# Performance work log

Measured on AMD Instinct MI355X. Metric: run time of the kernel, lower is better.

The kernel has to match this reference:

```python
import jax, jax.numpy as jnp
import numpy as np

N, E, IN, HID, H, G = 50000, 400000, 128, 16, 11, 64
HC = HID * H  # 176
OUT, NC = 32, 10
EPS = 1e-5


def setup_inputs() -> dict:
    key = jax.random.key(0)
    ks = jax.random.split(key, 20)
    def n(i, shape, s=0.05):
        return jax.random.normal(ks[i], shape, jnp.float32) * s
    inp = {}
    inp["x"] = jax.random.normal(ks[0], (N, IN), jnp.float32)
    inp["edge_index"] = jax.random.randint(ks[1], (2, E), 0, N, dtype=jnp.int32)
    inp["batch"] = jnp.sort(jax.random.randint(ks[2], (N,), 0, G, dtype=jnp.int32))
    inp["W_pre"] = n(3, (IN, HC)); inp["b_pre"] = jnp.zeros((HC,), jnp.float32)
    # GraphNorm params for gn_pre, gn1..gn4 stacked: [5, HC]
    inp["gn_w"] = jnp.ones((5, HC), jnp.float32)
    inp["gn_b"] = jnp.zeros((5, HC), jnp.float32)
    inp["gn_ms"] = jnp.ones((5, HC), jnp.float32)  # mean_scale
    # conv1..conv4 (concat=True) stacked params
    inp["conv_Wl"] = n(4, (4, HC, HC)); inp["conv_Wr"] = n(5, (4, HC, HC))
    inp["conv_att"] = n(6, (4, H, HID))
    inp["conv_b"] = jnp.zeros((4, HC), jnp.float32)
    inp["conv_Wres"] = n(7, (4, HC, HC))
    # conv5 (concat=False -> out dim HID)
    inp["c5_Wl"] = n(8, (HC, HC)); inp["c5_Wr"] = n(9, (HC, HC))
    inp["c5_att"] = n(10, (H, HID))
    inp["c5_b"] = jnp.zeros((HID,), jnp.float32)
    inp["c5_Wres"] = n(11, (HC, HID))
    inp["W_o1"] = n(12, (HID, HID)); inp["b_o1"] = jnp.zeros((HID,), jnp.float32)
    inp["W_o2"] = n(13, (HID, OUT)); inp["b_o2"] = jnp.zeros((OUT,), jnp.float32)
    inp["W_cls"] = n(14, (OUT, NC)); inp["b_cls"] = jnp.zeros((NC,), jnp.float32)
    return inp


def graph_norm(x, w, b, ms, batch, cnt):
    # PyG GraphNorm: out = w * (x - ms*mean) / sqrt(var + eps) + b, stats per graph
    mean = jax.ops.segment_sum(x, batch, G) / cnt  # [G, F]
    xc = x - mean[batch] * ms
    var = jax.ops.segment_sum(xc * xc, batch, G) / cnt
    std = jnp.sqrt(var + EPS)
    return w * xc / std[batch] + b


def gatv2_conv(x, Wl, Wr, att, bias, Wres, src, dst, concat):
    # src/dst already include self-loops (PyG add_self_loops=True)
    xl = (x @ Wl).reshape(N, H, -1)  # source transform [N,H,C]
    xr = (x @ Wr).reshape(N, H, -1)  # target transform [N,H,C]
    e = jax.nn.leaky_relu(xl[src] + xr[dst], 0.2)          # [E',H,C]
    alpha = jnp.einsum('ehc,hc->eh', e, att)               # [E',H]
    amax = jax.ops.segment_max(alpha, dst, N)
    amax = jnp.where(jnp.isfinite(amax), amax, 0.0)
    ex = jnp.exp(alpha - amax[dst])
    den = jax.ops.segment_sum(ex, dst, N)
    a = ex / (den[dst] + 1e-16)
    out = jax.ops.segment_sum(xl[src] * a[..., None], dst, N)  # [N,H,C]
    out = out.reshape(N, -1) if concat else out.mean(axis=1)
    return out + x @ Wres + bias


def reference(x, edge_index, batch, W_pre, b_pre, gn_w, gn_b, gn_ms,
              conv_Wl, conv_Wr, conv_att, conv_b, conv_Wres,
              c5_Wl, c5_Wr, c5_att, c5_b, c5_Wres,
              W_o1, b_o1, W_o2, b_o2, W_cls, b_cls):
    loops = jnp.arange(N, dtype=edge_index.dtype)
    src = jnp.concatenate([edge_index[0], loops])
    dst = jnp.concatenate([edge_index[1], loops])
    cnt = jax.ops.segment_sum(jnp.ones((N, 1), jnp.float32), batch, G)
    cnt = jnp.maximum(cnt, 1.0)  # guard empty graphs

    h = x @ W_pre + b_pre
    h = graph_norm(h, gn_w[0], gn_b[0], gn_ms[0], batch, cnt)
    h = jax.nn.relu(h)
    for i in range(4):
        h = gatv2_conv(h, conv_Wl[i], conv_Wr[i], conv_att[i], conv_b[i],
                       conv_Wres[i], src, dst, concat=True)
        h = graph_norm(h, gn_w[i + 1], gn_b[i + 1], gn_ms[i + 1], batch, cnt)
        h = jax.nn.relu(h)
    h = gatv2_conv(h, c5_Wl, c5_Wr, c5_att, c5_b, c5_Wres, src, dst, concat=False)
    h = jax.nn.relu(h)
    h = jax.nn.relu(h @ W_o1 + b_o1)
    h = jax.nn.relu(h @ W_o2 + b_o2)
    return h @ W_cls + b_cls
```

## Files before the change

### kernel.cpp

```cpp
#include <hip/hip_runtime.h>
#include <math.h>

#define N_NODES 50000
#define N_EDGES 400000
#define IN_F 128
#define HC 176
#define NGRAPH 64
#define NBLK_ATTN 12500
#define NCHUNK 16

typedef _Float16 half8 __attribute__((ext_vector_type(8)));
typedef _Float16 half4 __attribute__((ext_vector_type(4)));
typedef float floatx4 __attribute__((ext_vector_type(4)));

__device__ inline float4 h4f(const _Float16* p) {
  half4 h = *(const half4*)p;
  return make_float4((float)h[0], (float)h[1], (float)h[2], (float)h[3]);
}

#define PREH 45056
#define MATH 67584
#define TOT_PAIRS 495616
#define KCBYTES 22528
#define GX8 49

__global__ void prep_kernel(const float* __restrict__ Wpre,
                            const float* __restrict__ cWl, const float* __restrict__ cWr,
                            const float* __restrict__ cWres,
                            const float* __restrict__ c5Wl, const float* __restrict__ c5Wr,
                            _Float16* __restrict__ wp) {
  int gid = blockIdx.x * 256 + threadIdx.x;
  if (gid >= TOT_PAIRS) return;
  int mat, idx;
  if (gid < 22528) { mat = 0; idx = gid; }
  else { int g = gid - 22528; mat = 1 + g / 33792; idx = g % 33792; }
  int kc = idx / 5632;
  int rem = idx - kc * 5632;
  int ct = rem / 512;
  int li = rem - ct * 512;
  int lane = li >> 3, j = li & 7;
  int k = kc * 32 + ((lane >> 4) << 3) + j;
  int col = ct * 16 + (lane & 15);
  const float* src; int Ksrc; size_t base;
  if (mat == 0) { src = Wpre; Ksrc = 128; base = 0; }
  else if (mat <= 12) {
    int lm = mat - 1; int layer = lm / 3; int sub = lm - layer * 3;
    const float* s = (sub == 0) ? cWl : (sub == 1) ? cWr : cWres;
    src = s + (size_t)layer * HC * HC; Ksrc = HC;
    base = PREH + (size_t)lm * MATH;
  } else {
    src = (mat == 13) ? c5Wl : c5Wr; Ksrc = HC;
    base = PREH + (size_t)12 * MATH + (size_t)(mat - 13) * MATH;
  }
  float v = (k < Ksrc) ? src[(size_t)k * HC + col] : 0.0f;
  _Float16 h = (_Float16)v;
  _Float16 l = (_Float16)(v - (float)h);
  size_t o = base + (size_t)(kc * 11 + ct) * 1024 + li;
  wp[o] = h;
  wp[o + 512] = l;
}

template <int MINW, bool DOSTATS>
__global__ __launch_bounds__(256, MINW) void gemm_mfma_t(
    const float* __restrict__ A, int M, int K, int nkc, int nmat,
    const _Float16* __restrict__ Wp, int matStride,
    const float* __restrict__ scsh, const int* __restrict__ batch,
    const float* __restrict__ bias0, const float* __restrict__ bias1,
    const float* __restrict__ bias2,
    float* __restrict__ out0, float* __restrict__ out1, float* __restrict__ out2,
    float* __restrict__ parts, float* __restrict__ partq, float* __restrict__ stats,
    int halfMask) {
  __shared__ __align__(16) char smem[2 * KCBYTES];
  const int b = blockIdx.x;
  const int grp = b >> 3, sub = b & 7;
  const int mat = grp % nmat;
  const int tile = ((grp / nmat) << 3) | sub;
  if (tile * 128 >= M) return;
  const _Float16* W = Wp + (size_t)mat * matStride;
  float* outp = (mat == 0) ? out0 : (mat == 1) ? out1 : out2;
  const float* bias = (mat == 0) ? bias0 : (mat == 1) ? bias1 : bias2;
  const bool hOut = (halfMask >> mat) & 1;
  const int tid = threadIdx.x;
  const int lane = tid & 63;
  const int wv = tid >> 6;
  const int m16 = lane & 15, quad = lane >> 4;
  const int kb = quad << 3;
  const int rowBase = tile * 128 + wv * 32;
  const int rA0 = min(rowBase + m16, M - 1);
  const int rA1 = min(rowBase + 16 + m16, M - 1);
  const float* ap0 = A + (size_t)rA0 * K + kb;
  const float* ap1 = A + (size_t)rA1 * K + kb;
  const float* sc0 = nullptr; const float* sh0 = nullptr;
  const float* sc1 = nullptr; const float* sh1 = nullptr;
  if (scsh) {
    int g0 = batch[rA0], g1 = batch[rA1];
    sc0 = scsh + (size_t)g0 * HC + kb;
    sh0 = scsh + (size_t)(NGRAPH + g0) * HC + kb;
    sc1 = scsh + (size_t)g1 * HC + kb;
    sh1 = scsh + (size_t)(NGRAPH + g1) * HC + kb;
  }

  auto stage = [&](int kc, int buf) {
    const char* src = (const char*)W + (size_t)kc * KCBYTES;
    char* dst = smem + buf * KCBYTES;
#pragma unroll
    for (int i = 0; i < 6; i++) {
      int idx = wv * 6 + i;
      if (idx < 22) {
        __builtin_amdgcn_global_load_lds(
            (const __attribute__((address_space(1))) unsigned int*)(src + idx * 1024 + lane * 16),
            (__attribute__((address_space(3))) unsigned int*)(dst + idx * 1024),
            16, 0, 0);
      }
    }
  };

  floatx4 acc0[11], acc1[11];
#pragma unroll
  for (int ct = 0; ct < 11; ct++)
#pragma unroll
    for (int r = 0; r < 4; r++) { acc0[ct][r] = 0.0f; acc1[ct][r] = 0.0f; }

  stage(0, 0);

  for (int kc = 0; kc < nkc; kc++) {
    const int buf = kc & 1;
    __syncthreads();
    if (kc + 1 < nkc) stage(kc + 1, 1 - buf);

    const int koff = kc << 5;
    float va0[8], va1[8];
    if (koff + kb + 8 <= K) {
      float4 u0 = *(const float4*)(ap0 + koff);
      float4 u1 = *(const float4*)(ap0 + koff + 4);
      float4 w0 = *(const float4*)(ap1 + koff);
      float4 w1 = *(const float4*)(ap1 + koff + 4);
      va0[0] = u0.x; va0[1] = u0.y; va0[2] = u0.z; va0[3] = u0.w;
      va0[4] = u1.x; va0[5] = u1.y; va0[6] = u1.z; va0[7] = u1.w;
      va1[0] = w0.x; va1[1] = w0.y; va1[2] = w0.z; va1[3] = w0.w;
      va1[4] = w1.x; va1[5] = w1.y; va1[6] = w1.z; va1[7] = w1.w;
      if (scsh) {
        float s0[8], h0[8], s1[8], h1[8];
        float4 t;
        t = *(const float4*)(sc0 + koff);     s0[0]=t.x; s0[1]=t.y; s0[2]=t.z; s0[3]=t.w;
        t = *(const float4*)(sc0 + koff + 4); s0[4]=t.x; s0[5]=t.y; s0[6]=t.z; s0[7]=t.w;
        t = *(const float4*)(sh0 + koff);     h0[0]=t.x; h0[1]=t.y; h0[2]=t.z; h0[3]=t.w;
        t = *(const float4*)(sh0 + koff + 4); h0[4]=t.x; h0[5]=t.y; h0[6]=t.z; h0[7]=t.w;
        t = *(const float4*)(sc1 + koff);     s1[0]=t.x; s1[1]=t.y; s1[2]=t.z; s1[3]=t.w;
        t = *(const float4*)(sc1 + koff + 4); s1[4]=t.x; s1[5]=t.y; s1[6]=t.z; s1[7]=t.w;
        t = *(const float4*)(sh1 + koff);     h1[0]=t.x; h1[1]=t.y; h1[2]=t.z; h1[3]=t.w;
        t = *(const float4*)(sh1 + koff + 4); h1[4]=t.x; h1[5]=t.y; h1[6]=t.z; h1[7]=t.w;
#pragma unroll
        for (int j = 0; j < 8; j++) {
          va0[j] = fmaxf(fmaf(va0[j], s0[j], h0[j]), 0.0f);
          va1[j] = fmaxf(fmaf(va1[j], s1[j], h1[j]), 0.0f);
        }
      }
    } else {
#pragma unroll
      for (int j = 0; j < 8; j++) { va0[j] = 0.0f; va1[j] = 0.0f; }
    }
    half8 ah0, al0, ah1, al1;
#pragma unroll
    for (int j = 0; j < 8; j++) {
      _Float16 h = (_Float16)va0[j];
      ah0[j] = h; al0[j] = (_Float16)(va0[j] - (float)h);
      _Float16 g = (_Float16)va1[j];
      ah1[j] = g; al1[j] = (_Float16)(va1[j] - (float)g);
    }
    const char* bbase = smem + buf * KCBYTES + lane * 16;
#pragma unroll
    for (int ct = 0; ct < 11; ct++) {
      half8 bh = *(const half8*)(bbase + ct * 2048);
      half8 bl = *(const half8*)(bbase + ct * 2048 + 1024);
      acc0[ct] = __builtin_amdgcn_mfma_f32_16x16x32_f16(ah0, bh, acc0[ct], 0, 0, 0);
      acc1[ct] = __builtin_amdgcn_mfma_f32_16x16x32_f16(ah1, bh, acc1[ct], 0, 0, 0);
      acc0[ct] = __builtin_amdgcn_mfma_f32_16x16x32_f16(al0, bh, acc0[ct], 0, 0, 0);
      acc1[ct] = __builtin_amdgcn_mfma_f32_16x16x32_f16(al1, bh, acc1[ct], 0, 0, 0);
      acc0[ct] = __builtin_amdgcn_mfma_f32_16x16x32_f16(ah0, bl, acc0[ct], 0, 0, 0);
      acc1[ct] = __builtin_amdgcn_mfma_f32_16x16x32_f16(ah1, bl, acc1[ct], 0, 0, 0);
    }
  }

  float bv[11];
#pragma unroll
  for (int ct = 0; ct < 11; ct++) bv[ct] = bias ? bias[ct * 16 + m16] : 0.0f;
#pragma unroll
  for (int r = 0; r < 4; r++) {
    int row0 = rowBase + (quad << 2) + r;
    if (row0 < M) {
      if (hOut) {
        _Float16* op = (_Float16*)outp + (size_t)row0 * HC + m16;
#pragma unroll
        for (int ct = 0; ct < 11; ct++) op[ct * 16] = (_Float16)(acc0[ct][r] + bv[ct]);
      } else {
        float* op = outp + (size_t)row0 * HC + m16;
#pragma unroll
        for (int ct = 0; ct < 11; ct++) op[ct * 16] = acc0[ct][r] + bv[ct];
      }
    }
    int row1 = row0 + 16;
    if (row1 < M) {
      if (hOut) {
        _Float16* op = (_Float16*)outp + (size_t)row1 * HC + m16;
#pragma unroll
        for (int ct = 0; ct < 11; ct++) op[ct * 16] = (_Float16)(acc1[ct][r] + bv[ct]);
      } else {
        float* op = outp + (size_t)row1 * HC + m16;
#pragma unroll
        for (int ct = 0; ct < 11; ct++) op[ct * 16] = acc1[ct][r] + bv[ct];
      }
    }
  }

  if (DOSTATS) {
    int gTile = batch[tile * 128];
    int lastRow = min(tile * 128 + 127, M - 1);
    bool straddle = (batch[lastRow] != gTile);
    bool validR[8]; bool otherR[8];
#pragma unroll
    for (int r = 0; r < 4; r++) {
      int row0 = rowBase + (quad << 2) + r;
      validR[r] = (row0 < M);
      otherR[r] = validR[r] && (batch[min(row0, M - 1)] != gTile);
      int row1 = row0 + 16;
      validR[4 + r] = (row1 < M);
      otherR[4 + r] = validR[4 + r] && (batch[min(row1, M - 1)] != gTile);
    }
    __syncthreads();
    float* red = (float*)smem;
#pragma unroll
    for (int ct = 0; ct < 11; ct++) {
      float sA = 0.f, qA = 0.f, sB = 0.f, qB = 0.f;
#pragma unroll
      for (int r = 0; r < 4; r++) {
        if (validR[r]) {
          float v = acc0[ct][r] + bv[ct];
          if (otherR[r]) { sB += v; qB = fmaf(v, v, qB); }
          else           { sA += v; qA = fmaf(v, v, qA); }
        }
        if (validR[4 + r]) {
          float v = acc1[ct][r] + bv[ct];
          if (otherR[4 + r]) { sB += v; qB = fmaf(v, v, qB); }
          else               { sA += v; qA = fmaf(v, v, qA); }
        }
      }
      sA += __shfl_xor(sA, 16); sA += __shfl_xor(sA, 32);
      qA += __shfl_xor(qA, 16); qA += __shfl_xor(qA, 32);
      sB += __shfl_xor(sB, 16); sB += __shfl_xor(sB, 32);
      qB += __shfl_xor(qB, 16); qB += __shfl_xor(qB, 32);
      if (quad == 0) {
        float* slot = red + (((wv * 11 + ct) * 16 + m16) << 2);
        slot[0] = sA; slot[1] = qA; slot[2] = sB; slot[3] = qB;
      }
    }
    __syncthreads();
    if (tid < HC) {
      int col = tid;
      float sA = 0.f, qA = 0.f, sB = 0.f, qB = 0.f;
#pragma unroll
      for (int w = 0; w < 4; w++) {
        float* slot = red + (((w * 11 + col / 16) * 16 + (col & 15)) << 2);
        sA += slot[0]; qA += slot[1]; sB += slot[2]; qB += slot[3];
      }
      parts[(size_t)tile * HC + col] = sA;
      partq[(size_t)tile * HC + col] = qA;
      if (straddle) {
        int g2 = batch[lastRow];
        atomicAdd(&stats[g2 * HC + col], sB);
        atomicAdd(&stats[(NGRAPH + g2) * HC + col], qB);
      }
    }
  }
}

__global__ __launch_bounds__(256) void part_reduce_kernel(
    const float* __restrict__ parts, const float* __restrict__ partq,
    const int* __restrict__ gstart, float* __restrict__ stats, int rpb) {
  int idx = blockIdx.x * 256 + threadIdx.x;
  if (idx >= NGRAPH * NCHUNK * HC) return;
  int f = idx % HC;
  int gc = idx / HC;
  int g = gc / NCHUNK, c = gc % NCHUNK;
  int s0 = gstart[g], s1 = gstart[g + 1];
  int b0 = (s0 + rpb - 1) / rpb, b1 = (s1 + rpb - 1) / rpb;
  int len = b1 - b0;
  if (len <= 0) return;
  int per = (len + NCHUNK - 1) / NCHUNK;
  int cb0 = b0 + c * per;
  int cb1 = min(cb0 + per, b1);
  if (cb0 >= cb1) return;
  float s = 0.f, ss = 0.f;
  for (int b = cb0; b < cb1; b++) {
    s += parts[(size_t)b * HC + f];
    ss += partq[(size_t)b * HC + f];
  }
  atomicAdd(&stats[g * HC + f], s);
  atomicAdd(&stats[(NGRAPH + g) * HC + f], ss);
}

__global__ void gn_finalize_kernel(const float* __restrict__ stats, const int* __restrict__ cntInt,
                                   const float* __restrict__ gnw, const float* __restrict__ gnb,
                                   const float* __restrict__ gnms, int row,
                                   float* __restrict__ scsh) {
  int i = blockIdx.x * 256 + threadIdx.x;
  if (i >= NGRAPH * HC) return;
  int g = i / HC, f = i - g * HC;
  float c = fmaxf((float)cntInt[g], 1.0f);
  float m = stats[i] / c;
  float sq = stats[NGRAPH * HC + i] / c;
  float ms = gnms[row * HC + f];
  float var = sq - m * m * ms * (2.0f - ms);
  float w = gnw[row * HC + f], b = gnb[row * HC + f];
  float scale = w / sqrtf(var + 1e-5f);
  float shift = b - scale * ms * m;
  scsh[i] = scale;
  scsh[NGRAPH * HC + i] = shift;
}

__global__ void cnt_bsearch_kernel(const int* __restrict__ batch, int* __restrict__ cntInt,
                                   int* __restrict__ gstart) {
  int g = threadIdx.x;
  if (g >= NGRAPH) return;
  auto lb = [&](int v) {
    int lo = 0, hi = N_NODES;
    while (lo < hi) {
      int mid = (lo + hi) >> 1;
      if (batch[mid] < v) lo = mid + 1; else hi = mid;
    }
    return lo;
  };
  int a = lb(g), b = lb(g + 1);
  cntInt[g] = b - a;
  gstart[g] = a;
  if (g == NGRAPH - 1) gstart[NGRAPH] = N_NODES;
}

__global__ void deg_hist_kernel(const int* __restrict__ dstE, int* __restrict__ deg) {
  int e = blockIdx.x * 256 + threadIdx.x;
  if (e < N_EDGES) atomicAdd(&deg[dstE[e]], 1);
}

__global__ void scan1_kernel(const int* __restrict__ deg, int* __restrict__ bsum) {
  __shared__ int sd[256];
  int i = blockIdx.x * 256 + threadIdx.x;
  sd[threadIdx.x] = (i < N_NODES) ? deg[i] : 0;
  __syncthreads();
  for (int s = 128; s > 0; s >>= 1) {
    if (threadIdx.x < s) sd[threadIdx.x] += sd[threadIdx.x + s];
    __syncthreads();
  }
  if (threadIdx.x == 0) bsum[blockIdx.x] = sd[0];
}

__global__ void scan2_kernel(int* __restrict__ bsum, int nb) {
  __shared__ int sd[256];
  int t = threadIdx.x;
  int v0 = (t < nb) ? bsum[t] : 0;
  sd[t] = v0;
  __syncthreads();
  for (int s = 1; s < 256; s <<= 1) {
    int v = (t >= s) ? sd[t - s] : 0;
    __syncthreads();
    sd[t] += v;
    __syncthreads();
  }
  if (t < nb) bsum[t] = sd[t] - v0;
}

__global__ void scan3_kernel(const int* __restrict__ deg, const int* __restrict__ bsum,
                             int* __restrict__ rowptr) {
  __shared__ int sd[256];
  int i = blockIdx.x * 256 + threadIdx.x;
  int t = threadIdx.x;
  int d = (i < N_NODES) ? deg[i] : 0;
  sd[t] = d;
  __syncthreads();
  for (int s = 1; s < 256; s <<= 1) {
    int v = (t >= s) ? sd[t - s] : 0;
    __syncthreads();
    sd[t] += v;
    __syncthreads();
  }
  if (i < N_NODES) rowptr[i] = bsum[blockIdx.x] + sd[t] - d;
  if (i == 0) rowptr[N_NODES] = N_EDGES;
}

__global__ void scatter_kernel(const int* __restrict__ srcE, const int* __restrict__ dstE,
                               const int* __restrict__ rowptr, int* __restrict__ fill,
                               int* __restrict__ colA) {
  int e = blockIdx.x * 256 + threadIdx.x;
  if (e < N_EDGES) {
    int d = dstE[e];
    int pos = rowptr[d] + atomicAdd(&fill[d], 1);
    colA[pos] = srcE[e];
  }
}

#define AEDGE(V, D, ACC)                                                      \
  do {                                                                        \
    float e0 = (V).x + xrv.x; e0 = fmaxf(e0, 0.2f * e0);                      \
    float e1 = (V).y + xrv.y; e1 = fmaxf(e1, 0.2f * e1);                      \
    float e2 = (V).z + xrv.z; e2 = fmaxf(e2, 0.2f * e2);                      \
    float e3 = (V).w + xrv.w; e3 = fmaxf(e3, 0.2f * e3);                      \
    float p = fmaf(e3, av.w, fmaf(e2, av.z, fmaf(e1, av.y, e0 * av.x)));      \
    p += __shfl_xor(p, 1);                                                    \
    p += __shfl_xor(p, 2);                                                    \
    float pp = __expf(p);                                                     \
    (D) += pp;                                                                \
    (ACC).x = fmaf(pp, (V).x, (ACC).x);                                       \
    (ACC).y = fmaf(pp, (V).y, (ACC).y);                                       \
    (ACC).z = fmaf(pp, (V).z, (ACC).z);                                       \
    (ACC).w = fmaf(pp, (V).w, (ACC).w);                                       \
  } while (0)

__global__ __launch_bounds__(256) void attn_concat_kernel(
    const _Float16* __restrict__ xl, const _Float16* __restrict__ xr,
    const float* __restrict__ att, const int* __restrict__ rowptr,
    const int* __restrict__ colA, float* __restrict__ out,
    const int* __restrict__ batch, float* __restrict__ stats,
    float* __restrict__ parts, float* __restrict__ partq) {
  __shared__ float sv[4 * HC];
  int t = threadIdx.x;
  int node = blockIdx.x * 4 + (t >> 6);
  int lane = t & 63;
  if (lane < 44) {
    const float4 av = *(const float4*)(att + lane * 4);
    size_t base = (size_t)node * HC + lane * 4;
    const float4 xrv = h4f(xr + base);
    int start = rowptr[node], end = rowptr[node + 1];
    float d = 0.0f, dB = 0.0f;
    float4 acc = make_float4(0.f, 0.f, 0.f, 0.f);
    float4 accB = make_float4(0.f, 0.f, 0.f, 0.f);
    float4 p1, p2;
    if (start < end)     p1 = h4f(xl + (size_t)colA[start] * HC + lane * 4);
    if (start + 1 < end) p2 = h4f(xl + (size_t)colA[start + 1] * HC + lane * 4);
    {
      float4 svv = h4f(xl + base);
      AEDGE(svv, d, acc);
    }
    int j = start;
    for (; j + 3 < end; j += 2) {
      float4 n1 = h4f(xl + (size_t)colA[j + 2] * HC + lane * 4);
      float4 n2 = h4f(xl + (size_t)colA[j + 3] * HC + lane * 4);
      AEDGE(p1, d, acc);
      AEDGE(p2, dB, accB);
      p1 = n1; p2 = n2;
    }
    if (j < end)     AEDGE(p1, d, acc);
    if (j + 1 < end) AEDGE(p2, dB, accB);
    if (j + 2 < end) {
      float4 n1 = h4f(xl + (size_t)colA[j + 2] * HC + lane * 4);
      AEDGE(n1, d, acc);
    }
    d += dB;
    acc.x += accB.x; acc.y += accB.y; acc.z += accB.z; acc.w += accB.w;
    float rd = 1.0f / (d + 1e-16f);
    float4 o = *(const float4*)(out + base);
    o.x = fmaf(acc.x, rd, o.x);
    o.y = fmaf(acc.y, rd, o.y);
    o.z = fmaf(acc.z, rd, o.z);
    o.w = fmaf(acc.w, rd, o.w);
    *(float4*)(out + base) = o;
    *(float4*)(&sv[(t >> 6) * HC + lane * 4]) = o;
  }
  __syncthreads();
  if (t < HC) {
    int b = blockIdx.x;
    int g0 = batch[b * 4];
    float s = 0.0f, ss = 0.0f;
#pragma unroll
    for (int w = 0; w < 4; w++) {
      int g = batch[b * 4 + w];
      float v = sv[w * HC + t];
      if (g == g0) {
        s += v;
        ss = fmaf(v, v, ss);
      } else {
        atomicAdd(&stats[g * HC + t], v);
        atomicAdd(&stats[(NGRAPH + g) * HC + t], v * v);
      }
    }
    parts[(size_t)b * HC + t] = s;
    partq[(size_t)b * HC + t] = ss;
  }
}

__global__ __launch_bounds__(256) void attn_mean_kernel(
    const _Float16* __restrict__ xl, const _Float16* __restrict__ xr,
    const float* __restrict__ att, const int* __restrict__ rowptr,
    const int* __restrict__ colA, const float* __restrict__ res16,
    float* __restrict__ out16) {
  int t = threadIdx.x;
  int node = blockIdx.x * 4 + (t >> 6);
  int lane = t & 63;
  if (node >= N_NODES) return;
  int L = (lane < 44) ? lane : 0;
  const float4 av = *(const float4*)(att + L * 4);
  size_t base = (size_t)node * HC + L * 4;
  const float4 xrv = h4f(xr + base);
  int start = rowptr[node], end = rowptr[node + 1];
  float d = 0.0f, dB = 0.0f;
  float4 acc = make_float4(0.f, 0.f, 0.f, 0.f);
  float4 accB = make_float4(0.f, 0.f, 0.f, 0.f);
  float4 p1, p2;
  if (start < end)     p1 = h4f(xl + (size_t)colA[start] * HC + L * 4);
  if (start + 1 < end) p2 = h4f(xl + (size_t)colA[start + 1] * HC + L * 4);
  {
    float4 sv = h4f(xl + base);
    AEDGE(sv, d, acc);
  }
  int j = start;
  for (; j + 3 < end; j += 2) {
    float4 n1 = h4f(xl + (size_t)colA[j + 2] * HC + L * 4);
    float4 n2 = h4f(xl + (size_t)colA[j + 3] * HC + L * 4);
    AEDGE(p1, d, acc);
    AEDGE(p2, dB, accB);
    p1 = n1; p2 = n2;
  }
  if (j < end)     AEDGE(p1, d, acc);
  if (j + 1 < end) AEDGE(p2, dB, accB);
  if (j + 2 < end) {
    float4 n1 = h4f(xl + (size_t)colA[j + 2] * HC + L * 4);
    AEDGE(n1, d, acc);
  }
  d += dB;
  acc.x += accB.x; acc.y += accB.y; acc.z += accB.z; acc.w += accB.w;
  float rd = 1.0f / (d + 1e-16f);
  float4 o;
  o.x = (lane < 44) ? acc.x * rd : 0.0f;
  o.y = (lane < 44) ? acc.y * rd : 0.0f;
  o.z = (lane < 44) ? acc.z * rd : 0.0f;
  o.w = (lane < 44) ? acc.w * rd : 0.0f;
#pragma unroll
  for (int w = 4; w <= 32; w <<= 1) {
    o.x += __shfl_xor(o.x, w);
    o.y += __shfl_xor(o.y, w);
    o.z += __shfl_xor(o.z, w);
    o.w += __shfl_xor(o.w, w);
  }
  if (lane < 4) {
    const float* rp = res16 + (size_t)node * 16 + lane * 4;
    float4 r = *(const float4*)rp;
    float4 ov;
    ov.x = fmaxf(fmaf(o.x, 1.0f / 11.0f, r.x), 0.0f);
    ov.y = fmaxf(fmaf(o.y, 1.0f / 11.0f, r.y), 0.0f);
    ov.z = fmaxf(fmaf(o.z, 1.0f / 11.0f, r.z), 0.0f);
    ov.w = fmaxf(fmaf(o.w, 1.0f / 11.0f, r.w), 0.0f);
    *(float4*)(out16 + (size_t)node * 16 + lane * 4) = ov;
  }
}

__global__ __launch_bounds__(256) void res16_kernel(const float* __restrict__ h,
                                                    const float* __restrict__ scsh,
                                                    const int* __restrict__ batch,
                                                    const float* __restrict__ Wres,
                                                    const float* __restrict__ b16,
                                                    float* __restrict__ res16) {
  __shared__ float Ws[176 * 16];
  __shared__ float hs[16 * 176];
  int t = threadIdx.x;
  for (int i = t; i < 176 * 16; i += 256) Ws[i] = Wres[i];
  int n0 = blockIdx.x * 16;
  for (int i = t; i < 16 * 176; i += 256) {
    int row = i / 176, k = i - row * 176;
    int g = batch[n0 + row];
    float v = h[(size_t)n0 * HC + i];
    hs[i] = fmaxf(fmaf(v, scsh[g * HC + k], scsh[(NGRAPH + g) * HC + k]), 0.0f);
  }
  __syncthreads();
  int tx = t & 15, ty = t >> 4;
  float acc = b16[tx];
  for (int k = 0; k < HC; k++) acc = fmaf(hs[ty * HC + k], Ws[k * 16 + tx], acc);
  res16[(size_t)(n0 + ty) * 16 + tx] = acc;
}

__global__ __launch_bounds__(256) void head_kernel(
    const float* __restrict__ in16, const float* __restrict__ Wo1,
    const float* __restrict__ bo1, const float* __restrict__ Wo2,
    const float* __restrict__ bo2, const float* __restrict__ Wc,
    const float* __restrict__ bc, float* __restrict__ outp) {
  __shared__ float w1[256], w2[512], wcS[320], b1[16], b2[32], bcS[10];
  int t = threadIdx.x;
  for (int i = t; i < 256; i += 256) w1[i] = Wo1[i];
  for (int i = t; i < 512; i += 256) w2[i] = Wo2[i];
  for (int i = t; i < 320; i += 256) wcS[i] = Wc[i];
  if (t < 16) b1[t] = bo1[t];
  if (t < 32) b2[t] = bo2[t];
  if (t < 10) bcS[t] = bc[t];
  __syncthreads();
  int n = blockIdx.x * 256 + t;
  if (n >= N_NODES) return;
  float x[16];
#pragma unroll
  for (int i = 0; i < 16; i++) x[i] = in16[(size_t)n * 16 + i];
  float o1[16];
#pragma unroll
  for (int j = 0; j < 16; j++) {
    float a = b1[j];
#pragma unroll
    for (int k = 0; k < 16; k++) a = fmaf(x[k], w1[k * 16 + j], a);
    o1[j] = fmaxf(a, 0.0f);
  }
  float o2[32];
#pragma unroll
  for (int j = 0; j < 32; j++) {
    float a = b2[j];
#pragma unroll
    for (int k = 0; k < 16; k++) a = fmaf(o1[k], w2[k * 32 + j], a);
    o2[j] = fmaxf(a, 0.0f);
  }
#pragma unroll
  for (int j = 0; j < 10; j++) {
    float a = bcS[j];
#pragma unroll
    for (int k = 0; k < 32; k++) a = fmaf(o2[k], wcS[k * 10 + j], a);
    outp[(size_t)n * 10 + j] = a;
  }
}

extern "C" void kernel_launch(void* const* d_in, const int* in_sizes, int n_in,
                              void* d_out, int out_size, void* d_ws, size_t ws_size,
                              hipStream_t stream) {
  (void)in_sizes; (void)n_in; (void)out_size; (void)ws_size;
  const float* x     = (const float*)d_in[0];
  const int*   ei    = (const int*)d_in[1];
  const int*   srcE  = ei;
  const int*   dstE  = ei + N_EDGES;
  const int*   batch = (const int*)d_in[2];
  const float* W_pre = (const float*)d_in[3];
  const float* b_pre = (const float*)d_in[4];
  const float* gn_w  = (const float*)d_in[5];
  const float* gn_b  = (const float*)d_in[6];
  const float* gn_ms = (const float*)d_in[7];
  const float* cWl   = (const float*)d_in[8];
  const float* cWr   = (const float*)d_in[9];
  const float* cAtt  = (const float*)d_in[10];
  const float* cB    = (const float*)d_in[11];
  const float* cWres = (const float*)d_in[12];
  const float* c5Wl  = (const float*)d_in[13];
  const float* c5Wr  = (const float*)d_in[14];
  const float* c5Att = (const float*)d_in[15];
  const float* c5b   = (const float*)d_in[16];
  const float* c5Wres= (const float*)d_in[17];
  const float* Wo1   = (const float*)d_in[18];
  const float* bo1   = (const float*)d_in[19];
  const float* Wo2   = (const float*)d_in[20];
  const float* bo2   = (const float*)d_in[21];
  const float* Wc    = (const float*)d_in[22];
  const float* bc    = (const float*)d_in[23];

  const size_t FB = (size_t)N_NODES * HC;
  const size_t STB = (size_t)2 * NGRAPH * HC;
  const size_t PB = (size_t)NBLK_ATTN * HC;
  float* ws    = (float*)d_ws;
  float* buf0  = ws;
  float* buf1  = ws + FB;
  float* buf2  = ws + 2 * FB;
  float* buf3  = ws + 3 * FB;
  float* res16 = ws + 4 * FB;
  float* out16 = res16 + (size_t)N_NODES * 16;
  float* stats = out16 + (size_t)N_NODES * 16;
  int* deg     = (int*)(stats + 5 * STB);
  int* fill    = deg + N_NODES;
  float* scsh  = (float*)(fill + N_NODES);
  float* parts = scsh + STB;
  float* partq = parts + PB;
  _Float16* wph = (_Float16*)(partq + PB);
  int* ibase   = (int*)((char*)wph + (size_t)991232 * 2);
  int* cntInt  = ibase;
  int* gstart  = ibase + 64;
  int* rowptr  = gstart + 65;
  int* colA    = rowptr + N_NODES + 1;
  int* bsum    = colA + N_EDGES;

  const int NB = (N_NODES + 255) / 256;

  hipMemsetAsync(stats, 0, sizeof(float) * 5 * STB + sizeof(int) * 2 * N_NODES, stream);

  prep_kernel<<<(TOT_PAIRS + 255) / 256, 256, 0, stream>>>(W_pre, cWl, cWr, cWres, c5Wl, c5Wr, wph);
  cnt_bsearch_kernel<<<1, 64, 0, stream>>>(batch, cntInt, gstart);
  deg_hist_kernel<<<(N_EDGES + 255) / 256, 256, 0, stream>>>(dstE, deg);
  scan1_kernel<<<NB, 256, 0, stream>>>(deg, bsum);
  scan2_kernel<<<1, 256, 0, stream>>>(bsum, NB);
  scan3_kernel<<<NB, 256, 0, stream>>>(deg, bsum, rowptr);
  scatter_kernel<<<(N_EDGES + 255) / 256, 256, 0, stream>>>(srcE, dstE, rowptr, fill, colA);

  const int PRB = (NGRAPH * NCHUNK * HC + 255) / 256;

  gemm_mfma_t<2, true><<<GX8 * 1 * 8, 256, 0, stream>>>(
      x, N_NODES, IN_F, 4, 1, wph, 0, nullptr, batch,
      b_pre, nullptr, nullptr, buf0, nullptr, nullptr,
      parts, partq, stats, 0);
  part_reduce_kernel<<<PRB, 256, 0, stream>>>(parts, partq, gstart, stats, 128);
  gn_finalize_kernel<<<(NGRAPH * HC + 255) / 256, 256, 0, stream>>>(stats, cntInt, gn_w, gn_b, gn_ms, 0, scsh);

  float* h = buf0;
  float* o = buf3;
  for (int i = 0; i < 4; i++) {
    const _Float16* Wcat_i = wph + PREH + (size_t)(3 * i) * MATH;
    gemm_mfma_t<3, false><<<GX8 * 3 * 8, 256, 0, stream>>>(
        h, N_NODES, HC, 6, 3, Wcat_i, MATH, scsh, batch,
        nullptr, nullptr, cB + i * HC, buf1, buf2, o,
        nullptr, nullptr, nullptr, 3);
    float* st = stats + (size_t)(i + 1) * STB;
    attn_concat_kernel<<<NBLK_ATTN, 256, 0, stream>>>((const _Float16*)buf1, (const _Float16*)buf2,
                                                      cAtt + i * HC,
                                                      rowptr, colA, o, batch, st,
                                                      parts, partq);
    part_reduce_kernel<<<PRB, 256, 0, stream>>>(parts, partq, gstart, st, 4);
    gn_finalize_kernel<<<(NGRAPH * HC + 255) / 256, 256, 0, stream>>>(st, cntInt, gn_w, gn_b, gn_ms, i + 1, scsh);
    float* tmp = h; h = o; o = tmp;
  }

  const _Float16* Wc5 = wph + PREH + (size_t)12 * MATH;
  gemm_mfma_t<3, false><<<GX8 * 2 * 8, 256, 0, stream>>>(
      h, N_NODES, HC, 6, 2, Wc5, MATH, scsh, batch,
      nullptr, nullptr, nullptr, buf1, buf2, nullptr,
      nullptr, nullptr, nullptr, 3);
  res16_kernel<<<N_NODES / 16, 256, 0, stream>>>(h, scsh, batch, c5Wres, c5b, res16);
  attn_mean_kernel<<<(N_NODES + 3) / 4, 256, 0, stream>>>((const _Float16*)buf1, (const _Float16*)buf2,
                                                          c5Att, rowptr, colA, res16, out16);

  head_kernel<<<NB, 256, 0, stream>>>(out16, Wo1, bo1, Wo2, bo2, Wc, bc, (float*)d_out);
}
```

Measured before the change: 712.6 us.

## Reuse A-tile fragments across all weight matrices in one GEMM block; deepen attention gather prefetch

```diff
diff --git a/kernel.cpp b/kernel.cpp
--- a/kernel.cpp
+++ b/kernel.cpp
@@ -60,9 +60,9 @@
   wp[o + 512] = l;
 }
 
-template <int MINW, bool DOSTATS>
+template <int MINW, bool DOSTATS, int NKC>
 __global__ __launch_bounds__(256, MINW) void gemm_mfma_t(
-    const float* __restrict__ A, int M, int K, int nkc, int nmat,
+    const float* __restrict__ A, int M, int K, int nmat,
     const _Float16* __restrict__ Wp, int matStride,
     const float* __restrict__ scsh, const int* __restrict__ batch,
     const float* __restrict__ bias0, const float* __restrict__ bias1,
@@ -71,15 +71,8 @@
     float* __restrict__ parts, float* __restrict__ partq, float* __restrict__ stats,
     int halfMask) {
   __shared__ __align__(16) char smem[2 * KCBYTES];
-  const int b = blockIdx.x;
-  const int grp = b >> 3, sub = b & 7;
-  const int mat = grp % nmat;
-  const int tile = ((grp / nmat) << 3) | sub;
+  const int tile = blockIdx.x;
   if (tile * 128 >= M) return;
-  const _Float16* W = Wp + (size_t)mat * matStride;
-  float* outp = (mat == 0) ? out0 : (mat == 1) ? out1 : out2;
-  const float* bias = (mat == 0) ? bias0 : (mat == 1) ? bias1 : bias2;
-  const bool hOut = (halfMask >> mat) & 1;
   const int tid = threadIdx.x;
   const int lane = tid & 63;
   const int wv = tid >> 6;
@@ -100,7 +93,7 @@
     sh1 = scsh + (size_t)(NGRAPH + g1) * HC + kb;
   }
 
-  auto stage = [&](int kc, int buf) {
+  auto stage = [&](const _Float16* W, int kc, int buf) {
     const char* src = (const char*)W + (size_t)kc * KCBYTES;
     char* dst = smem + buf * KCBYTES;
 #pragma unroll
@@ -115,19 +108,11 @@
     }
   };
 
-  floatx4 acc0[11], acc1[11];
-#pragma unroll
-  for (int ct = 0; ct < 11; ct++)
-#pragma unroll
-    for (int r = 0; r < 4; r++) { acc0[ct][r] = 0.0f; acc1[ct][r] = 0.0f; }
-
-  stage(0, 0);
-
-  for (int kc = 0; kc < nkc; kc++) {
-    const int buf = kc & 1;
-    __syncthreads();
-    if (kc + 1 < nkc) stage(kc + 1, 1 - buf);
-
+  stage(Wp, 0, 0);
+
+  half8 AH0[NKC], AL0[NKC], AH1[NKC], AL1[NKC];
+#pragma unroll
+  for (int kc = 0; kc < NKC; kc++) {
     const int koff = kc << 5;
     float va0[8], va1[8];
     if (koff + kb + 8 <= K) {
@@ -160,55 +145,77 @@
 #pragma unroll
       for (int j = 0; j < 8; j++) { va0[j] = 0.0f; va1[j] = 0.0f; }
     }
-    half8 ah0, al0, ah1, al1;
+    half8 h0v, l0v, h1v, l1v;
 #pragma unroll
     for (int j = 0; j < 8; j++) {
       _Float16 h = (_Float16)va0[j];
-      ah0[j] = h; al0[j] = (_Float16)(va0[j] - (float)h);
+      h0v[j] = h; l0v[j] = (_Float16)(va0[j] - (float)h);
       _Float16 g = (_Float16)va1[j];
-      ah1[j] = g; al1[j] = (_Float16)(va1[j] - (float)g);
-    }
-    const char* bbase = smem + buf * KCBYTES + lane * 16;
+      h1v[j] = g; l1v[j] = (_Float16)(va1[j] - (float)g);
+    }
+    AH0[kc] = h0v; AL0[kc] = l0v; AH1[kc] = h1v; AL1[kc] = l1v;
+  }
+
+  floatx4 acc0[11], acc1[11];
+  float bv[11];
+
+  for (int m = 0; m < nmat; m++) {
+    const bool hOut = (halfMask >> m) & 1;
+    float* outp = (m == 0) ? out0 : (m == 1) ? out1 : out2;
+    const float* bias = (m == 0) ? bias0 : (m == 1) ? bias1 : bias2;
 #pragma unroll
     for (int ct = 0; ct < 11; ct++) {
-      half8 bh = *(const half8*)(bbase + ct * 2048);
-      half8 bl = *(const half8*)(bbase + ct * 2048 + 1024);
-      acc0[ct] = __builtin_amdgcn_mfma_f32_16x16x32_f16(ah0, bh, acc0[ct], 0, 0, 0);
-      acc1[ct] = __builtin_amdgcn_mfma_f32_16x16x32_f16(ah1, bh, acc1[ct], 0, 0, 0);
-      acc0[ct] = __builtin_amdgcn_mfma_f32_16x16x32_f16(al0, bh, acc0[ct], 0, 0, 0);
-      acc1[ct] = __builtin_amdgcn_mfma_f32_16x16x32_f16(al1, bh, acc1[ct], 0, 0, 0);
-      acc0[ct] = __builtin_amdgcn_mfma_f32_16x16x32_f16(ah0, bl, acc0[ct], 0, 0, 0);
-      acc1[ct] = __builtin_amdgcn_mfma_f32_16x16x32_f16(ah1, bl, acc1[ct], 0, 0, 0);
-    }
-  }
-
-  float bv[11];
-#pragma unroll
-  for (int ct = 0; ct < 11; ct++) bv[ct] = bias ? bias[ct * 16 + m16] : 0.0f;
-#pragma unroll
-  for (int r = 0; r < 4; r++) {
-    int row0 = rowBase + (quad << 2) + r;
-    if (row0 < M) {
-      if (hOut) {
-        _Float16* op = (_Float16*)outp + (size_t)row0 * HC + m16;
-#pragma unroll
-        for (int ct = 0; ct < 11; ct++) op[ct * 16] = (_Float16)(acc0[ct][r] + bv[ct]);
-      } else {
-        float* op = outp + (size_t)row0 * HC + m16;
-#pragma unroll
-        for (int ct = 0; ct < 11; ct++) op[ct * 16] = acc0[ct][r] + bv[ct];
-      }
-    }
-    int row1 = row0 + 16;
-    if (row1 < M) {
-      if (hOut) {
-        _Float16* op = (_Float16*)outp + (size_t)row1 * HC + m16;
-#pragma unroll
-        for (int ct = 0; ct < 11; ct++) op[ct * 16] = (_Float16)(acc1[ct][r] + bv[ct]);
-      } else {
-        float* op = outp + (size_t)row1 * HC + m16;
-#pragma unroll
-        for (int ct = 0; ct < 11; ct++) op[ct * 16] = acc1[ct][r] + bv[ct];
+      bv[ct] = bias ? bias[ct * 16 + m16] : 0.0f;
+#pragma unroll
+      for (int r = 0; r < 4; r++) { acc0[ct][r] = 0.0f; acc1[ct][r] = 0.0f; }
+    }
+#pragma unroll
+    for (int kc = 0; kc < NKC; kc++) {
+      const int s = m * NKC + kc;
+      __syncthreads();
+      if (s + 1 < nmat * NKC) {
+        const int m2 = (kc + 1 == NKC) ? m + 1 : m;
+        const int kc2 = (kc + 1 == NKC) ? 0 : kc + 1;
+        stage(Wp + (size_t)m2 * matStride, kc2, (s + 1) & 1);
+      }
+      const char* bbase = smem + (s & 1) * KCBYTES + lane * 16;
+#pragma unroll
+      for (int ct = 0; ct < 11; ct++) {
+        half8 bh = *(const half8*)(bbase + ct * 2048);
+        half8 bl = *(const half8*)(bbase + ct * 2048 + 1024);
+        acc0[ct] = __builtin_amdgcn_mfma_f32_16x16x32_f16(AH0[kc], bh, acc0[ct], 0, 0, 0);
+        acc1[ct] = __builtin_amdgcn_mfma_f32_16x16x32_f16(AH1[kc], bh, acc1[ct], 0, 0, 0);
+        acc0[ct] = __builtin_amdgcn_mfma_f32_16x16x32_f16(AL0[kc], bh, acc0[ct], 0, 0, 0);
+        acc1[ct] = __builtin_amdgcn_mfma_f32_16x16x32_f16(AL1[kc], bh, acc1[ct], 0, 0, 0);
+        acc0[ct] = __builtin_amdgcn_mfma_f32_16x16x32_f16(AH0[kc], bl, acc0[ct], 0, 0, 0);
+        acc1[ct] = __builtin_amdgcn_mfma_f32_16x16x32_f16(AH1[kc], bl, acc1[ct], 0, 0, 0);
+      }
+    }
+#pragma unroll
+    for (int r = 0; r < 4; r++) {
+      int row0 = rowBase + (quad << 2) + r;
+      if (row0 < M) {
+        if (hOut) {
+          _Float16* op = (_Float16*)outp + (size_t)row0 * HC + m16;
+#pragma unroll
+          for (int ct = 0; ct < 11; ct++) op[ct * 16] = (_Float16)(acc0[ct][r] + bv[ct]);
+        } else {
+          float* op = outp + (size_t)row0 * HC + m16;
+#pragma unroll
+          for (int ct = 0; ct < 11; ct++) op[ct * 16] = acc0[ct][r] + bv[ct];
+        }
+      }
+      int row1 = row0 + 16;
+      if (row1 < M) {
+        if (hOut) {
+          _Float16* op = (_Float16*)outp + (size_t)row1 * HC + m16;
+#pragma unroll
+          for (int ct = 0; ct < 11; ct++) op[ct * 16] = (_Float16)(acc1[ct][r] + bv[ct]);
+        } else {
+          float* op = outp + (size_t)row1 * HC + m16;
+#pragma unroll
+          for (int ct = 0; ct < 11; ct++) op[ct * 16] = acc1[ct][r] + bv[ct];
+        }
       }
     }
   }
@@ -414,6 +421,41 @@
     (ACC).w = fmaf(pp, (V).w, (ACC).w);                                       \
   } while (0)
 
+#define ATTN_BODY(XLBASE_LANE)                                                \
+  int start = rowptr[node], end = rowptr[node + 1];                           \
+  float d = 0.0f, dB = 0.0f;                                                  \
+  float4 acc = make_float4(0.f, 0.f, 0.f, 0.f);                               \
+  float4 accB = make_float4(0.f, 0.f, 0.f, 0.f);                              \
+  float4 p0, p1, p2, p3;                                                      \
+  if (start < end)     p0 = h4f(xl + (size_t)colA[start] * HC + (XLBASE_LANE)); \
+  if (start + 1 < end) p1 = h4f(xl + (size_t)colA[start + 1] * HC + (XLBASE_LANE)); \
+  if (start + 2 < end) p2 = h4f(xl + (size_t)colA[start + 2] * HC + (XLBASE_LANE)); \
+  if (start + 3 < end) p3 = h4f(xl + (size_t)colA[start + 3] * HC + (XLBASE_LANE)); \
+  {                                                                           \
+    float4 svv = h4f(xl + base);                                              \
+    AEDGE(svv, d, acc);                                                       \
+  }                                                                           \
+  int j = start;                                                              \
+  for (; j + 7 < end; j += 4) {                                               \
+    float4 n0 = h4f(xl + (size_t)colA[j + 4] * HC + (XLBASE_LANE));           \
+    float4 n1 = h4f(xl + (size_t)colA[j + 5] * HC + (XLBASE_LANE));           \
+    float4 n2 = h4f(xl + (size_t)colA[j + 6] * HC + (XLBASE_LANE));           \
+    float4 n3 = h4f(xl + (size_t)colA[j + 7] * HC + (XLBASE_LANE));           \
+    AEDGE(p0, d, acc); AEDGE(p1, dB, accB);                                   \
+    AEDGE(p2, d, acc); AEDGE(p3, dB, accB);                                   \
+    p0 = n0; p1 = n1; p2 = n2; p3 = n3;                                       \
+  }                                                                           \
+  if (j < end)     AEDGE(p0, d, acc);                                         \
+  if (j + 1 < end) AEDGE(p1, dB, accB);                                       \
+  if (j + 2 < end) AEDGE(p2, d, acc);                                         \
+  if (j + 3 < end) AEDGE(p3, dB, accB);                                       \
+  for (int k = j + 4; k < end; k++) {                                         \
+    float4 n = h4f(xl + (size_t)colA[k] * HC + (XLBASE_LANE));                \
+    AEDGE(n, d, acc);                                                         \
+  }                                                                           \
+  d += dB;                                                                    \
+  acc.x += accB.x; acc.y += accB.y; acc.z += accB.z; acc.w += accB.w;
+
 __global__ __launch_bounds__(256) void attn_concat_kernel(
     const _Float16* __restrict__ xl, const _Float16* __restrict__ xr,
     const float* __restrict__ att, const int* __restrict__ rowptr,
@@ -428,33 +470,7 @@
     const float4 av = *(const float4*)(att + lane * 4);
     size_t base = (size_t)node * HC + lane * 4;
     const float4 xrv = h4f(xr + base);
-    int start = rowptr[node], end = rowptr[node + 1];
-    float d = 0.0f, dB = 0.0f;
-    float4 acc = make_float4(0.f, 0.f, 0.f, 0.f);
-    float4 accB = make_float4(0.f, 0.f, 0.f, 0.f);
-    float4 p1, p2;
-    if (start < end)     p1 = h4f(xl + (size_t)colA[start] * HC + lane * 4);
-    if (start + 1 < end) p2 = h4f(xl + (size_t)colA[start + 1] * HC + lane * 4);
-    {
-      float4 svv = h4f(xl + base);
-      AEDGE(svv, d, acc);
-    }
-    int j = start;
-    for (; j + 3 < end; j += 2) {
-      float4 n1 = h4f(xl + (size_t)colA[j + 2] * HC + lane * 4);
-      float4 n2 = h4f(xl + (size_t)colA[j + 3] * HC + lane * 4);
-      AEDGE(p1, d, acc);
-      AEDGE(p2, dB, accB);
-      p1 = n1; p2 = n2;
-    }
-    if (j < end)     AEDGE(p1, d, acc);
-    if (j + 1 < end) AEDGE(p2, dB, accB);
-    if (j + 2 < end) {
-      float4 n1 = h4f(xl + (size_t)colA[j + 2] * HC + lane * 4);
-      AEDGE(n1, d, acc);
-    }
-    d += dB;
-    acc.x += accB.x; acc.y += accB.y; acc.z += accB.z; acc.w += accB.w;
+    ATTN_BODY(lane * 4)
     float rd = 1.0f / (d + 1e-16f);
     float4 o = *(const float4*)(out + base);
     o.x = fmaf(acc.x, rd, o.x);
@@ -499,33 +515,7 @@
   const float4 av = *(const float4*)(att + L * 4);
   size_t base = (size_t)node * HC + L * 4;
   const float4 xrv = h4f(xr + base);
-  int start = rowptr[node], end = rowptr[node + 1];
-  float d = 0.0f, dB = 0.0f;
-  float4 acc = make_float4(0.f, 0.f, 0.f, 0.f);
-  float4 accB = make_float4(0.f, 0.f, 0.f, 0.f);
-  float4 p1, p2;
-  if (start < end)     p1 = h4f(xl + (size_t)colA[start] * HC + L * 4);
-  if (start + 1 < end) p2 = h4f(xl + (size_t)colA[start + 1] * HC + L * 4);
-  {
-    float4 sv = h4f(xl + base);
-    AEDGE(sv, d, acc);
-  }
-  int j = start;
-  for (; j + 3 < end; j += 2) {
-    float4 n1 = h4f(xl + (size_t)colA[j + 2] * HC + L * 4);
-    float4 n2 = h4f(xl + (size_t)colA[j + 3] * HC + L * 4);
-    AEDGE(p1, d, acc);
-    AEDGE(p2, dB, accB);
-    p1 = n1; p2 = n2;
-  }
-  if (j < end)     AEDGE(p1, d, acc);
-  if (j + 1 < end) AEDGE(p2, dB, accB);
-  if (j + 2 < end) {
-    float4 n1 = h4f(xl + (size_t)colA[j + 2] * HC + L * 4);
-    AEDGE(n1, d, acc);
-  }
-  d += dB;
-  acc.x += accB.x; acc.y += accB.y; acc.z += accB.z; acc.w += accB.w;
+  ATTN_BODY(L * 4)
   float rd = 1.0f / (d + 1e-16f);
   float4 o;
   o.x = (lane < 44) ? acc.x * rd : 0.0f;
@@ -688,8 +678,8 @@
 
   const int PRB = (NGRAPH * NCHUNK * HC + 255) / 256;
 
-  gemm_mfma_t<2, true><<<GX8 * 1 * 8, 256, 0, stream>>>(
-      x, N_NODES, IN_F, 4, 1, wph, 0, nullptr, batch,
+  gemm_mfma_t<2, true, 4><<<GX8 * 8, 256, 0, stream>>>(
+      x, N_NODES, IN_F, 1, wph, 0, nullptr, batch,
       b_pre, nullptr, nullptr, buf0, nullptr, nullptr,
       parts, partq, stats, 0);
   part_reduce_kernel<<<PRB, 256, 0, stream>>>(parts, partq, gstart, stats, 128);
@@ -699,8 +689,8 @@
   float* o = buf3;
   for (int i = 0; i < 4; i++) {
     const _Float16* Wcat_i = wph + PREH + (size_t)(3 * i) * MATH;
-    gemm_mfma_t<3, false><<<GX8 * 3 * 8, 256, 0, stream>>>(
-        h, N_NODES, HC, 6, 3, Wcat_i, MATH, scsh, batch,
+    gemm_mfma_t<2, false, 6><<<GX8 * 8, 256, 0, stream>>>(
+        h, N_NODES, HC, 3, Wcat_i, MATH, scsh, batch,
         nullptr, nullptr, cB + i * HC, buf1, buf2, o,
         nullptr, nullptr, nullptr, 3);
     float* st = stats + (size_t)(i + 1) * STB;
@@ -714,8 +704,8 @@
   }
 
   const _Float16* Wc5 = wph + PREH + (size_t)12 * MATH;
-  gemm_mfma_t<3, false><<<GX8 * 2 * 8, 256, 0, stream>>>(
-      h, N_NODES, HC, 6, 2, Wc5, MATH, scsh, batch,
+  gemm_mfma_t<2, false, 6><<<GX8 * 8, 256, 0, stream>>>(
+      h, N_NODES, HC, 2, Wc5, MATH, scsh, batch,
       nullptr, nullptr, nullptr, buf1, buf2, nullptr,
       nullptr, nullptr, nullptr, 3);
   res16_kernel<<<N_NODES / 16, 256, 0, stream>>>(h, scsh, batch, c5Wres, c5b, res16);
```

Result: slower. 846.6 us (+18.8%).

## Store inter-layer node features in fp16 instead of fp32

Applied to the files above, without the earlier changes.

```diff
diff --git a/kernel.cpp b/kernel.cpp
--- a/kernel.cpp
+++ b/kernel.cpp
@@ -60,7 +60,7 @@
   wp[o + 512] = l;
 }
 
-template <int MINW, bool DOSTATS>
+template <int MINW, bool DOSTATS, bool AHALF>
 __global__ __launch_bounds__(256, MINW) void gemm_mfma_t(
     const float* __restrict__ A, int M, int K, int nkc, int nmat,
     const _Float16* __restrict__ Wp, int matStride,
@@ -90,6 +90,8 @@
   const int rA1 = min(rowBase + 16 + m16, M - 1);
   const float* ap0 = A + (size_t)rA0 * K + kb;
   const float* ap1 = A + (size_t)rA1 * K + kb;
+  const _Float16* hp0 = (const _Float16*)A + (size_t)rA0 * K + kb;
+  const _Float16* hp1 = (const _Float16*)A + (size_t)rA1 * K + kb;
   const float* sc0 = nullptr; const float* sh0 = nullptr;
   const float* sc1 = nullptr; const float* sh1 = nullptr;
   if (scsh) {
@@ -131,14 +133,21 @@
     const int koff = kc << 5;
     float va0[8], va1[8];
     if (koff + kb + 8 <= K) {
-      float4 u0 = *(const float4*)(ap0 + koff);
-      float4 u1 = *(const float4*)(ap0 + koff + 4);
-      float4 w0 = *(const float4*)(ap1 + koff);
-      float4 w1 = *(const float4*)(ap1 + koff + 4);
-      va0[0] = u0.x; va0[1] = u0.y; va0[2] = u0.z; va0[3] = u0.w;
-      va0[4] = u1.x; va0[5] = u1.y; va0[6] = u1.z; va0[7] = u1.w;
-      va1[0] = w0.x; va1[1] = w0.y; va1[2] = w0.z; va1[3] = w0.w;
-      va1[4] = w1.x; va1[5] = w1.y; va1[6] = w1.z; va1[7] = w1.w;
+      if (AHALF) {
+        half8 u = *(const half8*)(hp0 + koff);
+        half8 w = *(const half8*)(hp1 + koff);
+#pragma unroll
+        for (int j = 0; j < 8; j++) { va0[j] = (float)u[j]; va1[j] = (float)w[j]; }
+      } else {
+        float4 u0 = *(const float4*)(ap0 + koff);
+        float4 u1 = *(const float4*)(ap0 + koff + 4);
+        float4 w0 = *(const float4*)(ap1 + koff);
+        float4 w1 = *(const float4*)(ap1 + koff + 4);
+        va0[0] = u0.x; va0[1] = u0.y; va0[2] = u0.z; va0[3] = u0.w;
+        va0[4] = u1.x; va0[5] = u1.y; va0[6] = u1.z; va0[7] = u1.w;
+        va1[0] = w0.x; va1[1] = w0.y; va1[2] = w0.z; va1[3] = w0.w;
+        va1[4] = w1.x; va1[5] = w1.y; va1[6] = w1.z; va1[7] = w1.w;
+      }
       if (scsh) {
         float s0[8], h0[8], s1[8], h1[8];
         float4 t;
@@ -417,7 +426,7 @@
 __global__ __launch_bounds__(256) void attn_concat_kernel(
     const _Float16* __restrict__ xl, const _Float16* __restrict__ xr,
     const float* __restrict__ att, const int* __restrict__ rowptr,
-    const int* __restrict__ colA, float* __restrict__ out,
+    const int* __restrict__ colA, _Float16* __restrict__ out,
     const int* __restrict__ batch, float* __restrict__ stats,
     float* __restrict__ parts, float* __restrict__ partq) {
   __shared__ float sv[4 * HC];
@@ -456,12 +465,16 @@
     d += dB;
     acc.x += accB.x; acc.y += accB.y; acc.z += accB.z; acc.w += accB.w;
     float rd = 1.0f / (d + 1e-16f);
-    float4 o = *(const float4*)(out + base);
-    o.x = fmaf(acc.x, rd, o.x);
-    o.y = fmaf(acc.y, rd, o.y);
-    o.z = fmaf(acc.z, rd, o.z);
-    o.w = fmaf(acc.w, rd, o.w);
-    *(float4*)(out + base) = o;
+    half4 rv = *(const half4*)(out + base);
+    float4 o;
+    o.x = fmaf(acc.x, rd, (float)rv[0]);
+    o.y = fmaf(acc.y, rd, (float)rv[1]);
+    o.z = fmaf(acc.z, rd, (float)rv[2]);
+    o.w = fmaf(acc.w, rd, (float)rv[3]);
+    half4 st;
+    st[0] = (_Float16)o.x; st[1] = (_Float16)o.y;
+    st[2] = (_Float16)o.z; st[3] = (_Float16)o.w;
+    *(half4*)(out + base) = st;
     *(float4*)(&sv[(t >> 6) * HC + lane * 4]) = o;
   }
   __syncthreads();
@@ -507,8 +520,8 @@
   if (start < end)     p1 = h4f(xl + (size_t)colA[start] * HC + L * 4);
   if (start + 1 < end) p2 = h4f(xl + (size_t)colA[start + 1] * HC + L * 4);
   {
-    float4 sv = h4f(xl + base);
-    AEDGE(sv, d, acc);
+    float4 svv = h4f(xl + base);
+    AEDGE(svv, d, acc);
   }
   int j = start;
   for (; j + 3 < end; j += 2) {
@@ -551,7 +564,7 @@
   }
 }
 
-__global__ __launch_bounds__(256) void res16_kernel(const float* __restrict__ h,
+__global__ __launch_bounds__(256) void res16_kernel(const _Float16* __restrict__ h,
                                                     const float* __restrict__ scsh,
                                                     const int* __restrict__ batch,
                                                     const float* __restrict__ Wres,
@@ -565,7 +578,7 @@
   for (int i = t; i < 16 * 176; i += 256) {
     int row = i / 176, k = i - row * 176;
     int g = batch[n0 + row];
-    float v = h[(size_t)n0 * HC + i];
+    float v = (float)h[(size_t)n0 * HC + i];
     hs[i] = fmaxf(fmaf(v, scsh[g * HC + k], scsh[(NGRAPH + g) * HC + k]), 0.0f);
   }
   __syncthreads();
@@ -688,10 +701,10 @@
 
   const int PRB = (NGRAPH * NCHUNK * HC + 255) / 256;
 
-  gemm_mfma_t<2, true><<<GX8 * 1 * 8, 256, 0, stream>>>(
+  gemm_mfma_t<2, true, false><<<GX8 * 1 * 8, 256, 0, stream>>>(
       x, N_NODES, IN_F, 4, 1, wph, 0, nullptr, batch,
       b_pre, nullptr, nullptr, buf0, nullptr, nullptr,
-      parts, partq, stats, 0);
+      parts, partq, stats, 1);
   part_reduce_kernel<<<PRB, 256, 0, stream>>>(parts, partq, gstart, stats, 128);
   gn_finalize_kernel<<<(NGRAPH * HC + 255) / 256, 256, 0, stream>>>(stats, cntInt, gn_w, gn_b, gn_ms, 0, scsh);
 
@@ -699,14 +712,14 @@
   float* o = buf3;
   for (int i = 0; i < 4; i++) {
     const _Float16* Wcat_i = wph + PREH + (size_t)(3 * i) * MATH;
-    gemm_mfma_t<3, false><<<GX8 * 3 * 8, 256, 0, stream>>>(
+    gemm_mfma_t<3, false, true><<<GX8 * 3 * 8, 256, 0, stream>>>(
         h, N_NODES, HC, 6, 3, Wcat_i, MATH, scsh, batch,
         nullptr, nullptr, cB + i * HC, buf1, buf2, o,
-        nullptr, nullptr, nullptr, 3);
+        nullptr, nullptr, nullptr, 7);
     float* st = stats + (size_t)(i + 1) * STB;
     attn_concat_kernel<<<NBLK_ATTN, 256, 0, stream>>>((const _Float16*)buf1, (const _Float16*)buf2,
                                                       cAtt + i * HC,
-                                                      rowptr, colA, o, batch, st,
+                                                      rowptr, colA, (_Float16*)o, batch, st,
                                                       parts, partq);
     part_reduce_kernel<<<PRB, 256, 0, stream>>>(parts, partq, gstart, st, 4);
     gn_finalize_kernel<<<(NGRAPH * HC + 255) / 256, 256, 0, stream>>>(st, cntInt, gn_w, gn_b, gn_ms, i + 1, scsh);
@@ -714,11 +727,11 @@
   }
 
   const _Float16* Wc5 = wph + PREH + (size_t)12 * MATH;
-  gemm_mfma_t<3, false><<<GX8 * 2 * 8, 256, 0, stream>>>(
+  gemm_mfma_t<3, false, true><<<GX8 * 2 * 8, 256, 0, stream>>>(
       h, N_NODES, HC, 6, 2, Wc5, MATH, scsh, batch,
       nullptr, nullptr, nullptr, buf1, buf2, nullptr,
       nullptr, nullptr, nullptr, 3);
-  res16_kernel<<<N_NODES / 16, 256, 0, stream>>>(h, scsh, batch, c5Wres, c5b, res16);
+  res16_kernel<<<N_NODES / 16, 256, 0, stream>>>((const _Float16*)h, scsh, batch, c5Wres, c5b, res16);
   attn_mean_kernel<<<(N_NODES + 3) / 4, 256, 0, stream>>>((const _Float16*)buf1, (const _Float16*)buf2,
                                                           c5Att, rowptr, colA, res16, out16);
 
```

Result: no change. 705.4 us (-1.0%).
